# Kernel tuning notes

Measured on AMD Instinct MI355X. Metric: run time of the kernel, lower is better.

## Reference

```python
import jax, jax.numpy as jnp
import numpy as np

B, NCOL, NCOND = 1024, 64, 64
NRODT, D, NEST, NFOREST, NHID, NCLASS = 1024, 4, 128, 100, 128, 10
EPS = 1e-5


def setup_inputs() -> dict:
    key = jax.random.key(0)
    ks = jax.random.split(key, 16)
    rng = np.random.default_rng(0)
    s = 0.1
    inp = {
        'x': jax.random.normal(ks[0], (B, NCOL), jnp.float32),
        # phi_1 numerical grouped conv: groups=NCOL, in_per_g=1, out_per_g=NCOND
        'w1': jax.random.normal(ks[1], (NCOL, 1, NCOND), jnp.float32) * s,
        'b1': jax.random.normal(ks[2], (NCOL * NCOND,), jnp.float32) * s,
        # rODTConstruction fixed permutation of the 4096 conditions
        'perm': jnp.asarray(rng.permutation(NCOND * NCOL), jnp.int32),
        'gn1_g': jnp.ones((NCOND * NCOL,), jnp.float32),
        'gn1_b': jnp.zeros((NCOND * NCOL,), jnp.float32),
        # phi_2 grouped convs: groups=NRODT, block D->D then D->1
        'w2a': jax.random.normal(ks[3], (NRODT, D, D), jnp.float32) * s,
        'b2a': jax.random.normal(ks[4], (NRODT * D,), jnp.float32) * s,
        'gn2_g': jnp.ones((NCOND * NCOL,), jnp.float32),
        'gn2_b': jnp.zeros((NCOND * NCOL,), jnp.float32),
        'w2b': jax.random.normal(ks[5], (NRODT, D, 1), jnp.float32) * s,
        'b2b': jax.random.normal(ks[6], (NRODT,), jnp.float32) * s,
        'E': jax.random.normal(ks[7], (NRODT, NHID), jnp.float32) * s,
        # eval-mode sample_without_replacement buffer: per-forest subset of rODTs
        'swr': jnp.asarray(np.argsort(rng.random((NFOREST, NRODT)), axis=-1)[:, :NEST], jnp.int32),
        'ln1_g': jnp.ones((NHID,), jnp.float32),
        'ln1_b': jnp.zeros((NHID,), jnp.float32),
        'lin1_w': jax.random.normal(ks[8], (NHID, NHID), jnp.float32) * s,
        'lin1_b': jax.random.normal(ks[9], (NHID,), jnp.float32) * s,
        'ln2_g': jnp.ones((NHID,), jnp.float32),
        'ln2_b': jnp.zeros((NHID,), jnp.float32),
        'lin2_w': jax.random.normal(ks[10], (NHID, NCLASS), jnp.float32) * s,
        'lin2_b': jax.random.normal(ks[11], (NCLASS,), jnp.float32) * s,
    }
    return inp


def _group_norm(v, g, gamma, beta):
    # v: (B, C), normalize within each of g channel groups (L=1 in the torch module)
    b, c = v.shape
    vg = v.reshape(b, g, c // g)
    mu = vg.mean(-1, keepdims=True)
    var = vg.var(-1, keepdims=True)
    vn = ((vg - mu) / jnp.sqrt(var + EPS)).reshape(b, c)
    return vn * gamma + beta


def _layer_norm(v, gamma, beta):
    mu = v.mean(-1, keepdims=True)
    var = v.var(-1, keepdims=True)
    return (v - mu) / jnp.sqrt(var + EPS) * gamma + beta


def reference(x, w1, b1, perm, gn1_g, gn1_b, w2a, b2a, gn2_g, gn2_b, w2b, b2b,
              E, swr, ln1_g, ln1_b, lin1_w, lin1_b, ln2_g, ln2_b, lin2_w, lin2_b):
    b = x.shape[0]
    # ConditionGeneration (numerical only): block-diag GEMV with in_per_group=1
    M = jax.nn.sigmoid(x[:, :, None] * w1[None, :, 0, :] + b1.reshape(NCOL, NCOND))  # (B, NCOL, NCOND)
    M = M.transpose(0, 2, 1)  # (B, NCOND, NCOL)
    # rODTConstruction: flatten + fixed permutation
    O = M.reshape(b, NCOND * NCOL)[:, perm]  # (B, 4096)
    # phi_2: GroupNorm -> grouped conv (D->D) -> ReLU -> GroupNorm -> grouped conv (D->1)
    h = _group_norm(O, NRODT, gn1_g, gn1_b).reshape(b, NRODT, D)
    h = jnp.einsum('bgi,gio->bgo', h, w2a) + b2a.reshape(NRODT, D)
    h = jax.nn.relu(h).reshape(b, NRODT * D)
    h = _group_norm(h, NRODT, gn2_g, gn2_b).reshape(b, NRODT, D)
    w = jnp.einsum('bgi,gio->bgo', h, w2b)[..., 0] + b2b  # (B, NRODT), n_head=1
    # forest construction: gather rODT subsets, softmax over estimators, weighted embed sum
    ws = jax.nn.softmax(w[:, swr], axis=-1)  # (B, NFOREST, NEST)
    Es = E[swr]  # (NFOREST, NEST, NHID)
    F = jnp.einsum('bfe,feh->bfh', ws, Es)  # (B, NFOREST, NHID)
    # phi_3 bagging MLP (eval mode: dropout = identity)
    z = _layer_norm(F, ln1_g, ln1_b)
    z = jax.nn.relu(z @ lin1_w + lin1_b)
    z = _layer_norm(z, ln2_g, ln2_b)
    y_hats = z @ lin2_w + lin2_b  # (B, NFOREST, NCLASS)
    return y_hats.mean(1)  # (B, NCLASS)
```

## Files before the change

kernel.cpp:

```cpp
#include <hip/hip_runtime.h>


#define B_      1024
#define NCOL_   64
#define NCOND_  64
#define NRODT_  1024
#define NEST_   128
#define NFOREST_ 100
#define NHID_   128
#define NCLASS_ 10
#define EPS_    1e-5f

typedef __bf16 bf16_t;
typedef bf16_t bf16x8 __attribute__((ext_vector_type(8)));
typedef float  f32x4  __attribute__((ext_vector_type(4)));

#define MFMA16(a,b,c) __builtin_amdgcn_mfma_f32_16x16x32_bf16(a,b,c,0,0,0)

#define EG_FRAGS   (NFOREST_*4*8*64)
#define W1_FRAGS   (4*8*64)
#define L2_FRAGS   (4*64)

#define ZLD 136

__global__ __launch_bounds__(256) void k_prep(
    const float* __restrict__ E,     const int*   __restrict__ swr,
    const float* __restrict__ lin1w, const float* __restrict__ lin2w,
    const float* __restrict__ x,     const float* __restrict__ lin2b,
    bf16_t* __restrict__ Eh,  bf16_t* __restrict__ El,
    bf16_t* __restrict__ Wh,  bf16_t* __restrict__ Wl,
    bf16_t* __restrict__ L2h, bf16_t* __restrict__ L2l,
    float*  __restrict__ x_t, float* __restrict__ out)
{
    int blk = blockIdx.x, tid = threadIdx.x;
    if (blk < 800) {
        int t = blk * 256 + tid;
        int lane = t & 63, nn = (t >> 6) & 7, kk = (t >> 9) & 3, f = t >> 11;
        int q = lane >> 4, n = nn * 16 + (lane & 15);
        bf16x8 hi, lo;
#pragma unroll
        for (int j = 0; j < 8; ++j) {
            int e = kk * 32 + q * 8 + j;
            int r = swr[f * NEST_ + e];
            float v = E[r * NHID_ + n];
            bf16_t h = (bf16_t)v;
            hi[j] = h; lo[j] = (bf16_t)(v - (float)h);
        }
        *(bf16x8*)(Eh + (size_t)t * 8) = hi;
        *(bf16x8*)(El + (size_t)t * 8) = lo;
    } else if (blk < 808) {
        int t = (blk - 800) * 256 + tid;
        int lane = t & 63, nn = (t >> 6) & 7, kk = t >> 9;
        int q = lane >> 4, n = nn * 16 + (lane & 15);
        bf16x8 hi, lo;
#pragma unroll
        for (int j = 0; j < 8; ++j) {
            int k = kk * 32 + q * 8 + j;
            float v = lin1w[k * NHID_ + n];
            bf16_t h = (bf16_t)v;
            hi[j] = h; lo[j] = (bf16_t)(v - (float)h);
        }
        *(bf16x8*)(Wh + t * 8) = hi;
        *(bf16x8*)(Wl + t * 8) = lo;
    } else if (blk == 808) {
        int t = tid;
        int lane = t & 63, kk = t >> 6;
        int q = lane >> 4, n = lane & 15;
        bf16x8 hi, lo;
#pragma unroll
        for (int j = 0; j < 8; ++j) {
            int k = kk * 32 + q * 8 + j;
            float v = (n < NCLASS_) ? lin2w[k * NCLASS_ + n] : 0.f;
            bf16_t h = (bf16_t)v;
            hi[j] = h; lo[j] = (bf16_t)(v - (float)h);
        }
        *(bf16x8*)(L2h + t * 8) = hi;
        *(bf16x8*)(L2l + t * 8) = lo;
    } else if (blk < 1065) {
        int t = (blk - 809) * 256 + tid;
        x_t[t] = x[(t & 1023) * NCOL_ + (t >> 10)];
    } else {
        int t = (blk - 1065) * 256 + tid;
        if (t < B_ * NCLASS_) out[t] = lin2b[t % NCLASS_];
    }
}

__global__ __launch_bounds__(256) void k_rodt(
    const float* __restrict__ x_t,  const float* __restrict__ w1,
    const float* __restrict__ b1,   const int*  __restrict__ perm,
    const float* __restrict__ gn1g, const float* __restrict__ gn1b,
    const float* __restrict__ w2a,  const float* __restrict__ b2a,
    const float* __restrict__ gn2g, const float* __restrict__ gn2b,
    const float* __restrict__ w2b,  const float* __restrict__ b2b,
    float* __restrict__ w_t)
{
    int g  = blockIdx.x;
    int bq = threadIdx.x * 4;

    int4 p4 = ((const int4*)perm)[g];
    int col[4]  = { p4.x & 63, p4.y & 63, p4.z & 63, p4.w & 63 };
    int cond[4] = { p4.x >> 6, p4.y >> 6, p4.z >> 6, p4.w >> 6 };
    float w1v[4], b1v[4];
#pragma unroll
    for (int j = 0; j < 4; ++j) {
        w1v[j] = w1[col[j] * NCOND_ + cond[j]];
        b1v[j] = b1[col[j] * NCOND_ + cond[j]];
    }
    float4 g1  = ((const float4*)gn1g)[g];
    float4 o1  = ((const float4*)gn1b)[g];
    float4 ba  = ((const float4*)b2a)[g];
    float4 g2  = ((const float4*)gn2g)[g];
    float4 o2  = ((const float4*)gn2b)[g];
    float4 wb4 = ((const float4*)w2b)[g];
    float  bb  = b2b[g];
    float4 wa[4];
    const float4* w2a4 = (const float4*)w2a;
#pragma unroll
    for (int i = 0; i < 4; ++i) wa[i] = w2a4[g * 4 + i];

    float xv[4][4];
#pragma unroll
    for (int j = 0; j < 4; ++j) {
        float4 t = *(const float4*)&x_t[col[j] * B_ + bq];
        xv[j][0] = t.x; xv[j][1] = t.y; xv[j][2] = t.z; xv[j][3] = t.w;
    }

    float outv[4];
#pragma unroll
    for (int bi = 0; bi < 4; ++bi) {
        float v[4];
#pragma unroll
        for (int j = 0; j < 4; ++j) {
            float t = xv[j][bi] * w1v[j] + b1v[j];
            v[j] = 1.0f / (1.0f + __expf(-t));
        }
        float mu = (v[0] + v[1] + v[2] + v[3]) * 0.25f;
        float var = 0.f;
#pragma unroll
        for (int j = 0; j < 4; ++j) { float d = v[j] - mu; var += d * d; }
        var *= 0.25f;
        float rs = rsqrtf(var + EPS_);
        float h[4];
        h[0] = (v[0] - mu) * rs * g1.x + o1.x;
        h[1] = (v[1] - mu) * rs * g1.y + o1.y;
        h[2] = (v[2] - mu) * rs * g1.z + o1.z;
        h[3] = (v[3] - mu) * rs * g1.w + o1.w;

        float4 a = ba;
#pragma unroll
        for (int i = 0; i < 4; ++i) {
            a.x += h[i] * wa[i].x; a.y += h[i] * wa[i].y;
            a.z += h[i] * wa[i].z; a.w += h[i] * wa[i].w;
        }
        float t2[4];
        t2[0] = fmaxf(a.x, 0.f); t2[1] = fmaxf(a.y, 0.f);
        t2[2] = fmaxf(a.z, 0.f); t2[3] = fmaxf(a.w, 0.f);

        float mu2 = (t2[0] + t2[1] + t2[2] + t2[3]) * 0.25f;
        float var2 = 0.f;
#pragma unroll
        for (int j = 0; j < 4; ++j) { float d = t2[j] - mu2; var2 += d * d; }
        var2 *= 0.25f;
        float rs2 = rsqrtf(var2 + EPS_);

        float wvv = bb;
        wvv += ((t2[0] - mu2) * rs2 * g2.x + o2.x) * wb4.x;
        wvv += ((t2[1] - mu2) * rs2 * g2.y + o2.y) * wb4.y;
        wvv += ((t2[2] - mu2) * rs2 * g2.z + o2.z) * wb4.z;
        wvv += ((t2[3] - mu2) * rs2 * g2.w + o2.w) * wb4.w;
        outv[bi] = wvv;
    }
    *(float4*)&w_t[(size_t)g * B_ + bq] = make_float4(outv[0], outv[1], outv[2], outv[3]);
}

__global__ __launch_bounds__(256, 3) void k_forest(
    const float*  __restrict__ w_t, const int* __restrict__ swr,
    const bf16_t* __restrict__ Eh,  const bf16_t* __restrict__ El,
    const bf16_t* __restrict__ Wh,  const bf16_t* __restrict__ Wl,
    const bf16_t* __restrict__ L2h, const bf16_t* __restrict__ L2l,
    const float* __restrict__ ln1g, const float* __restrict__ ln1b,
    const float* __restrict__ lin1b,
    const float* __restrict__ ln2g, const float* __restrict__ ln2b,
    float* __restrict__ out)
{
    __shared__ __align__(16) float  zC[64 * 132];
    __shared__ __align__(16) bf16_t zb[64 * ZLD];

    int tid  = threadIdx.x;
    int wid  = tid >> 6;
    int lane = tid & 63;
    int q    = lane >> 4;
    int mc   = lane & 15;

    int n    = blockIdx.x;
    int swiz = (n & 7) * 200 + (n >> 3);
    int f    = swiz >> 4;
    int bt   = swiz & 15;
    int b0   = bt * 64 + wid * 16;

    const int* swrf = swr + f * NEST_;
    int nn0 = wid * 2;

    const bf16x8* EHf = (const bf16x8*)Eh;
    const bf16x8* ELf = (const bf16x8*)El;
    const bf16x8* WHf = (const bf16x8*)Wh;
    const bf16x8* WLf = (const bf16x8*)Wl;
    const bf16x8* LHf = (const bf16x8*)L2h;
    const bf16x8* LLf = (const bf16x8*)L2l;

    float ex[4][8];
    float mx = -1e30f;
#pragma unroll
    for (int kk = 0; kk < 4; ++kk) {
        int4 r0 = *(const int4*)(swrf + kk * 32 + q * 8);
        int4 r1 = *(const int4*)(swrf + kk * 32 + q * 8 + 4);
        int rr[8] = { r0.x, r0.y, r0.z, r0.w, r1.x, r1.y, r1.z, r1.w };
#pragma unroll
        for (int j = 0; j < 8; ++j) {
            float v = w_t[rr[j] * B_ + b0 + mc];
            ex[kk][j] = v;
            mx = fmaxf(mx, v);
        }
    }

    bf16x8 pe[4][4];
#pragma unroll
    for (int kk = 0; kk < 4; ++kk) {
        size_t bi = (size_t)(f * 4 + kk) * 8;
        pe[kk][0] = EHf[(bi + nn0) * 64 + lane];
        pe[kk][1] = EHf[(bi + nn0 + 1) * 64 + lane];
        pe[kk][2] = ELf[(bi + nn0) * 64 + lane];
        pe[kk][3] = ELf[(bi + nn0 + 1) * 64 + lane];
    }

    mx = fmaxf(mx, __shfl_xor(mx, 16));
    mx = fmaxf(mx, __shfl_xor(mx, 32));
    float s = 0.f;
#pragma unroll
    for (int kk = 0; kk < 4; ++kk)
#pragma unroll
        for (int j = 0; j < 8; ++j) { ex[kk][j] = __expf(ex[kk][j] - mx); s += ex[kk][j]; }
    s += __shfl_xor(s, 16);
    s += __shfl_xor(s, 32);
    float inv = 1.f / s;

#pragma unroll
    for (int kk = 0; kk < 4; ++kk) {
        bf16x8 v;
#pragma unroll
        for (int j = 0; j < 8; ++j) v[j] = (bf16_t)(ex[kk][j] * inv);
        *(bf16x8*)&zb[(wid * 16 + mc) * ZLD + kk * 32 + q * 8] = v;
    }

    __syncthreads();

    f32x4 accF[4][2];
#pragma unroll
    for (int mt = 0; mt < 4; ++mt) {
        accF[mt][0] = (f32x4){0.f, 0.f, 0.f, 0.f};
        accF[mt][1] = (f32x4){0.f, 0.f, 0.f, 0.f};
    }
#pragma unroll
    for (int kk = 0; kk < 4; ++kk) {
        bf16x8 av[4];
#pragma unroll
        for (int mt = 0; mt < 4; ++mt)
            av[mt] = *(const bf16x8*)&zb[(mt * 16 + mc) * ZLD + kk * 32 + q * 8];
#pragma unroll
        for (int mt = 0; mt < 4; ++mt) {
            accF[mt][0] = MFMA16(av[mt], pe[kk][0], accF[mt][0]);
            accF[mt][1] = MFMA16(av[mt], pe[kk][1], accF[mt][1]);
            accF[mt][0] = MFMA16(av[mt], pe[kk][2], accF[mt][0]);
            accF[mt][1] = MFMA16(av[mt], pe[kk][3], accF[mt][1]);
        }
    }

    bf16x8 pw[4][4];
#pragma unroll
    for (int kk = 0; kk < 4; ++kk) {
        pw[kk][0] = WHf[(kk * 8 + nn0) * 64 + lane];
        pw[kk][1] = WHf[(kk * 8 + nn0 + 1) * 64 + lane];
        pw[kk][2] = WLf[(kk * 8 + nn0) * 64 + lane];
        pw[kk][3] = WLf[(kk * 8 + nn0 + 1) * 64 + lane];
    }

#pragma unroll
    for (int mt = 0; mt < 4; ++mt)
#pragma unroll
        for (int nj = 0; nj < 2; ++nj)
#pragma unroll
            for (int reg = 0; reg < 4; ++reg)
                zC[(mt * 16 + q * 4 + reg) * 132 + (nn0 + nj) * 16 + mc] = accF[mt][nj][reg];

    __syncthreads();

    {
        float vv[8][4];
#pragma unroll
        for (int nn = 0; nn < 8; ++nn)
#pragma unroll
            for (int reg = 0; reg < 4; ++reg)
                vv[nn][reg] = zC[(wid * 16 + q * 4 + reg) * 132 + nn * 16 + mc];
        float mu[4], rs[4];
#pragma unroll
        for (int reg = 0; reg < 4; ++reg) {
            float ps = 0.f, pq = 0.f;
#pragma unroll
            for (int nn = 0; nn < 8; ++nn) { float v = vv[nn][reg]; ps += v; pq += v * v; }
#pragma unroll
            for (int o = 1; o <= 8; o <<= 1) { ps += __shfl_xor(ps, o); pq += __shfl_xor(pq, o); }
            float m_ = ps * (1.f / NHID_);
            mu[reg] = m_;
            rs[reg] = rsqrtf(pq * (1.f / NHID_) - m_ * m_ + EPS_);
        }
#pragma unroll
        for (int nn = 0; nn < 8; ++nn) {
            int c = nn * 16 + mc;
            float gv = ln1g[c], bv = ln1b[c];
#pragma unroll
            for (int reg = 0; reg < 4; ++reg)
                zb[(wid * 16 + q * 4 + reg) * ZLD + c] =
                    (bf16_t)((vv[nn][reg] - mu[reg]) * rs[reg] * gv + bv);
        }
    }

    __syncthreads();

    f32x4 accA[4][2];
#pragma unroll
    for (int mt = 0; mt < 4; ++mt) {
        accA[mt][0] = (f32x4){0.f, 0.f, 0.f, 0.f};
        accA[mt][1] = (f32x4){0.f, 0.f, 0.f, 0.f};
    }
#pragma unroll
    for (int kk = 0; kk < 4; ++kk) {
        bf16x8 av[4];
#pragma unroll
        for (int mt = 0; mt < 4; ++mt)
            av[mt] = *(const bf16x8*)&zb[(mt * 16 + mc) * ZLD + kk * 32 + q * 8];
#pragma unroll
        for (int mt = 0; mt < 4; ++mt) {
            accA[mt][0] = MFMA16(av[mt], pw[kk][0], accA[mt][0]);
            accA[mt][1] = MFMA16(av[mt], pw[kk][1], accA[mt][1]);
            accA[mt][0] = MFMA16(av[mt], pw[kk][2], accA[mt][0]);
            accA[mt][1] = MFMA16(av[mt], pw[kk][3], accA[mt][1]);
        }
    }

    __syncthreads();
#pragma unroll
    for (int mt = 0; mt < 4; ++mt)
#pragma unroll
        for (int nj = 0; nj < 2; ++nj)
#pragma unroll
            for (int reg = 0; reg < 4; ++reg)
                zC[(mt * 16 + q * 4 + reg) * 132 + (nn0 + nj) * 16 + mc] = accA[mt][nj][reg];

    bf16x8 pl2[4][2];
#pragma unroll
    for (int kk = 0; kk < 4; ++kk) {
        pl2[kk][0] = LHf[kk * 64 + lane];
        pl2[kk][1] = LLf[kk * 64 + lane];
    }

    __syncthreads();

    {
        float vv[8][4];
#pragma unroll
        for (int nn = 0; nn < 8; ++nn) {
            float bv = lin1b[nn * 16 + mc];
#pragma unroll
            for (int reg = 0; reg < 4; ++reg)
                vv[nn][reg] = fmaxf(
                    zC[(wid * 16 + q * 4 + reg) * 132 + nn * 16 + mc] + bv, 0.f);
        }
        float mu2[4], rs2[4];
#pragma unroll
        for (int reg = 0; reg < 4; ++reg) {
            float ps = 0.f, pq = 0.f;
#pragma unroll
            for (int nn = 0; nn < 8; ++nn) { float v = vv[nn][reg]; ps += v; pq += v * v; }
#pragma unroll
            for (int o = 1; o <= 8; o <<= 1) { ps += __shfl_xor(ps, o); pq += __shfl_xor(pq, o); }
            float m_ = ps * (1.f / NHID_);
            mu2[reg] = m_;
            rs2[reg] = rsqrtf(pq * (1.f / NHID_) - m_ * m_ + EPS_);
        }
#pragma unroll
        for (int nn = 0; nn < 8; ++nn) {
            int c = nn * 16 + mc;
            float gv = ln2g[c], bv = ln2b[c];
#pragma unroll
            for (int reg = 0; reg < 4; ++reg)
                zb[(wid * 16 + q * 4 + reg) * ZLD + c] =
                    (bf16_t)((vv[nn][reg] - mu2[reg]) * rs2[reg] * gv + bv);
        }
    }

    f32x4 accO = {0.f, 0.f, 0.f, 0.f};
#pragma unroll
    for (int kk = 0; kk < 4; ++kk) {
        bf16x8 a3 = *(const bf16x8*)&zb[(wid * 16 + mc) * ZLD + kk * 32 + q * 8];
        accO = MFMA16(a3, pl2[kk][0], accO);
        accO = MFMA16(a3, pl2[kk][1], accO);
    }
    if (mc < NCLASS_) {
#pragma unroll
        for (int reg = 0; reg < 4; ++reg)
            atomicAdd(&out[(b0 + q * 4 + reg) * NCLASS_ + mc],
                      accO[reg] * (1.f / NFOREST_));
    }
}

extern "C" void kernel_launch(void* const* d_in, const int* in_sizes, int n_in,
                              void* d_out, int out_size, void* d_ws, size_t ws_size,
                              hipStream_t stream)
{
    const float* x     = (const float*)d_in[0];
    const float* w1    = (const float*)d_in[1];
    const float* b1    = (const float*)d_in[2];
    const int*   perm  = (const int*)  d_in[3];
    const float* gn1g  = (const float*)d_in[4];
    const float* gn1b  = (const float*)d_in[5];
    const float* w2a   = (const float*)d_in[6];
    const float* b2a   = (const float*)d_in[7];
    const float* gn2g  = (const float*)d_in[8];
    const float* gn2b  = (const float*)d_in[9];
    const float* w2b   = (const float*)d_in[10];
    const float* b2b   = (const float*)d_in[11];
    const float* E     = (const float*)d_in[12];
    const int*   swr   = (const int*)  d_in[13];
    const float* ln1g  = (const float*)d_in[14];
    const float* ln1b  = (const float*)d_in[15];
    const float* lin1w = (const float*)d_in[16];
    const float* lin1b = (const float*)d_in[17];
    const float* ln2g  = (const float*)d_in[18];
    const float* ln2b  = (const float*)d_in[19];
    const float* lin2w = (const float*)d_in[20];
    const float* lin2b = (const float*)d_in[21];

    char* base = (char*)d_ws;
    float*  w_t  = (float*)base;
    float*  x_t  = (float*)(base + 4u * 1024 * 1024 + 64 * 1024);
    bf16_t* Eh   = (bf16_t*)(base + 4u * 1024 * 1024 + 64 * 1024 + 256 * 1024);
    bf16_t* El   = Eh  + (size_t)EG_FRAGS * 8;
    bf16_t* Wh   = El  + (size_t)EG_FRAGS * 8;
    bf16_t* Wl   = Wh  + (size_t)W1_FRAGS * 8;
    bf16_t* L2h  = Wl  + (size_t)W1_FRAGS * 8;
    bf16_t* L2l  = L2h + (size_t)L2_FRAGS * 8;

    k_prep<<<1105, 256, 0, stream>>>(E, swr, lin1w, lin2w, x, lin2b,
                                     Eh, El, Wh, Wl, L2h, L2l, x_t,
                                     (float*)d_out);

    k_rodt<<<NRODT_, 256, 0, stream>>>(
        x_t, w1, b1, perm, gn1g, gn1b, w2a, b2a, gn2g, gn2b, w2b, b2b, w_t);

    k_forest<<<NFOREST_ * 16, 256, 0, stream>>>(
        w_t, swr, Eh, El, Wh, Wl, L2h, L2l,
        ln1g, ln1b, lin1b, ln2g, ln2b, (float*)d_out);
}
```

Baseline: 138.5 us.

## Compute LayerNorm stats in registers via per-wave partials, drop fp32 LDS staging

Removes the 33KB fp32 zC shared buffer that held MFMA outputs for the two LayerNorms. Each wave now reduces the sum and sum of squares of its own column slice with shuffles and writes small float2 partials to a tiny shared array. All waves then combine the partials and normalize their own accumulator registers directly into the bf16 operand buffer. The smaller LDS footprint lets launch bounds rise from 3 to 4 blocks per CU, adding an extra barrier before the final MFMA and raising register pressure as the trade-off.

```diff
diff --git a/kernel.cpp b/kernel.cpp
--- a/kernel.cpp
+++ b/kernel.cpp
@@ -173,7 +173,7 @@
     *(float4*)&w_t[(size_t)g * B_ + bq] = make_float4(outv[0], outv[1], outv[2], outv[3]);
 }
 
-__global__ __launch_bounds__(256, 3) void k_forest(
+__global__ __launch_bounds__(256, 4) void k_forest(
     const float*  __restrict__ w_t, const int* __restrict__ swr,
     const bf16_t* __restrict__ Eh,  const bf16_t* __restrict__ El,
     const bf16_t* __restrict__ Wh,  const bf16_t* __restrict__ Wl,
@@ -183,8 +183,8 @@
     const float* __restrict__ ln2g, const float* __restrict__ ln2b,
     float* __restrict__ out)
 {
-    __shared__ __align__(16) float  zC[64 * 132];
     __shared__ __align__(16) bf16_t zb[64 * ZLD];
+    __shared__ __align__(8)  float2 pstat[4][64];
 
     int tid  = threadIdx.x;
     int wid  = tid >> 6;
@@ -275,6 +275,18 @@
         }
     }
 
+#pragma unroll
+    for (int mt = 0; mt < 4; ++mt)
+#pragma unroll
+        for (int reg = 0; reg < 4; ++reg) {
+            float a0 = accF[mt][0][reg], a1 = accF[mt][1][reg];
+            float sp = a0 + a1;
+            float qp = a0 * a0 + a1 * a1;
+#pragma unroll
+            for (int o = 1; o <= 8; o <<= 1) { sp += __shfl_xor(sp, o); qp += __shfl_xor(qp, o); }
+            if (mc == 0) pstat[wid][mt * 16 + q * 4 + reg] = make_float2(sp, qp);
+        }
+
     bf16x8 pw[4][4];
 #pragma unroll
     for (int kk = 0; kk < 4; ++kk) {
@@ -284,44 +296,27 @@
         pw[kk][3] = WLf[(kk * 8 + nn0 + 1) * 64 + lane];
     }
 
-#pragma unroll
-    for (int mt = 0; mt < 4; ++mt)
-#pragma unroll
-        for (int nj = 0; nj < 2; ++nj)
-#pragma unroll
-            for (int reg = 0; reg < 4; ++reg)
-                zC[(mt * 16 + q * 4 + reg) * 132 + (nn0 + nj) * 16 + mc] = accF[mt][nj][reg];
-
     __syncthreads();
 
     {
-        float vv[8][4];
-#pragma unroll
-        for (int nn = 0; nn < 8; ++nn)
-#pragma unroll
-            for (int reg = 0; reg < 4; ++reg)
-                vv[nn][reg] = zC[(wid * 16 + q * 4 + reg) * 132 + nn * 16 + mc];
-        float mu[4], rs[4];
-#pragma unroll
-        for (int reg = 0; reg < 4; ++reg) {
-            float ps = 0.f, pq = 0.f;
-#pragma unroll
-            for (int nn = 0; nn < 8; ++nn) { float v = vv[nn][reg]; ps += v; pq += v * v; }
-#pragma unroll
-            for (int o = 1; o <= 8; o <<= 1) { ps += __shfl_xor(ps, o); pq += __shfl_xor(pq, o); }
-            float m_ = ps * (1.f / NHID_);
-            mu[reg] = m_;
-            rs[reg] = rsqrtf(pq * (1.f / NHID_) - m_ * m_ + EPS_);
-        }
-#pragma unroll
-        for (int nn = 0; nn < 8; ++nn) {
-            int c = nn * 16 + mc;
-            float gv = ln1g[c], bv = ln1b[c];
-#pragma unroll
-            for (int reg = 0; reg < 4; ++reg)
-                zb[(wid * 16 + q * 4 + reg) * ZLD + c] =
-                    (bf16_t)((vv[nn][reg] - mu[reg]) * rs[reg] * gv + bv);
-        }
+        float gv0 = ln1g[nn0 * 16 + mc],      bv0 = ln1b[nn0 * 16 + mc];
+        float gv1 = ln1g[nn0 * 16 + 16 + mc], bv1 = ln1b[nn0 * 16 + 16 + mc];
+#pragma unroll
+        for (int mt = 0; mt < 4; ++mt)
+#pragma unroll
+            for (int reg = 0; reg < 4; ++reg) {
+                int r = mt * 16 + q * 4 + reg;
+                float2 p0 = pstat[0][r], p1 = pstat[1][r];
+                float2 p2 = pstat[2][r], p3 = pstat[3][r];
+                float sv = (p0.x + p1.x) + (p2.x + p3.x);
+                float qv = (p0.y + p1.y) + (p2.y + p3.y);
+                float m_ = sv * (1.f / NHID_);
+                float rv = rsqrtf(qv * (1.f / NHID_) - m_ * m_ + EPS_);
+                zb[r * ZLD + nn0 * 16 + mc] =
+                    (bf16_t)((accF[mt][0][reg] - m_) * rv * gv0 + bv0);
+                zb[r * ZLD + nn0 * 16 + 16 + mc] =
+                    (bf16_t)((accF[mt][1][reg] - m_) * rv * gv1 + bv1);
+            }
     }
 
     __syncthreads();
@@ -347,14 +342,28 @@
         }
     }
 
-    __syncthreads();
+    {
+        float bb0 = lin1b[nn0 * 16 + mc];
+        float bb1 = lin1b[nn0 * 16 + 16 + mc];
+#pragma unroll
+        for (int mt = 0; mt < 4; ++mt)
+#pragma unroll
+            for (int reg = 0; reg < 4; ++reg) {
+                accA[mt][0][reg] = fmaxf(accA[mt][0][reg] + bb0, 0.f);
+                accA[mt][1][reg] = fmaxf(accA[mt][1][reg] + bb1, 0.f);
+            }
+    }
 #pragma unroll
     for (int mt = 0; mt < 4; ++mt)
 #pragma unroll
-        for (int nj = 0; nj < 2; ++nj)
-#pragma unroll
-            for (int reg = 0; reg < 4; ++reg)
-                zC[(mt * 16 + q * 4 + reg) * 132 + (nn0 + nj) * 16 + mc] = accA[mt][nj][reg];
+        for (int reg = 0; reg < 4; ++reg) {
+            float a0 = accA[mt][0][reg], a1 = accA[mt][1][reg];
+            float sp = a0 + a1;
+            float qp = a0 * a0 + a1 * a1;
+#pragma unroll
+            for (int o = 1; o <= 8; o <<= 1) { sp += __shfl_xor(sp, o); qp += __shfl_xor(qp, o); }
+            if (mc == 0) pstat[wid][mt * 16 + q * 4 + reg] = make_float2(sp, qp);
+        }
 
     bf16x8 pl2[4][2];
 #pragma unroll
@@ -366,37 +375,27 @@
     __syncthreads();
 
     {
-        float vv[8][4];
-#pragma unroll
-        for (int nn = 0; nn < 8; ++nn) {
-            float bv = lin1b[nn * 16 + mc];
-#pragma unroll
-            for (int reg = 0; reg < 4; ++reg)
-                vv[nn][reg] = fmaxf(
-                    zC[(wid * 16 + q * 4 + reg) * 132 + nn * 16 + mc] + bv, 0.f);
-        }
-        float mu2[4], rs2[4];
-#pragma unroll
-        for (int reg = 0; reg < 4; ++reg) {
-            float ps = 0.f, pq = 0.f;
-#pragma unroll
-            for (int nn = 0; nn < 8; ++nn) { float v = vv[nn][reg]; ps += v; pq += v * v; }
-#pragma unroll
-            for (int o = 1; o <= 8; o <<= 1) { ps += __shfl_xor(ps, o); pq += __shfl_xor(pq, o); }
-            float m_ = ps * (1.f / NHID_);
-            mu2[reg] = m_;
-            rs2[reg] = rsqrtf(pq * (1.f / NHID_) - m_ * m_ + EPS_);
-        }
-#pragma unroll
-        for (int nn = 0; nn < 8; ++nn) {
-            int c = nn * 16 + mc;
-            float gv = ln2g[c], bv = ln2b[c];
-#pragma unroll
-            for (int reg = 0; reg < 4; ++reg)
-                zb[(wid * 16 + q * 4 + reg) * ZLD + c] =
-                    (bf16_t)((vv[nn][reg] - mu2[reg]) * rs2[reg] * gv + bv);
-        }
-    }
+        float gv0 = ln2g[nn0 * 16 + mc],      bv0 = ln2b[nn0 * 16 + mc];
+        float gv1 = ln2g[nn0 * 16 + 16 + mc], bv1 = ln2b[nn0 * 16 + 16 + mc];
+#pragma unroll
+        for (int mt = 0; mt < 4; ++mt)
+#pragma unroll
+            for (int reg = 0; reg < 4; ++reg) {
+                int r = mt * 16 + q * 4 + reg;
+                float2 p0 = pstat[0][r], p1 = pstat[1][r];
+                float2 p2 = pstat[2][r], p3 = pstat[3][r];
+                float sv = (p0.x + p1.x) + (p2.x + p3.x);
+                float qv = (p0.y + p1.y) + (p2.y + p3.y);
+                float m_ = sv * (1.f / NHID_);
+                float rv = rsqrtf(qv * (1.f / NHID_) - m_ * m_ + EPS_);
+                zb[r * ZLD + nn0 * 16 + mc] =
+                    (bf16_t)((accA[mt][0][reg] - m_) * rv * gv0 + bv0);
+                zb[r * ZLD + nn0 * 16 + 16 + mc] =
+                    (bf16_t)((accA[mt][1][reg] - m_) * rv * gv1 + bv1);
+            }
+    }
+
+    __syncthreads();
 
     f32x4 accO = {0.f, 0.f, 0.f, 0.f};
 #pragma unroll
```

New measurement: 151.6 us. +9.4%, slower.
